# Optimization experiments

Hardware: AMD Instinct MI355X
Metric: run time of the kernel (lower is better)

## Reference

```python
import jax, jax.numpy as jnp
import numpy as np

B, H, S, D = 4, 16, 2048, 64
TEMPERATURE = 8.0  # sqrt(D)
MASK_FILL = -1e9


def setup_inputs() -> dict:
    key = jax.random.key(0)
    kq, kk, kv, km = jax.random.split(key, 4)
    q = jax.random.normal(kq, (B, H, S, D), dtype=jnp.float32)
    k = jax.random.normal(kk, (B, H, S, D), dtype=jnp.float32)
    v = jax.random.normal(kv, (B, H, S, D), dtype=jnp.float32)
    mask = jax.random.randint(km, (B, 1, 1, S), 0, 2, dtype=jnp.int32)
    return {"q": q, "k": k, "v": v, "mask": mask}


def reference(q, k, v, mask):
    # attn = (q / temperature) @ k^T  -> [B,H,S,S]
    attn = jnp.einsum('bhqd,bhkd->bhqk', q / TEMPERATURE, k)
    # mask-fill where mask == 0 (broadcasts over heads/query dim)
    attn = jnp.where(mask == 0, MASK_FILL, attn)
    # dropout is identity at inference (training=None in the original)
    # NOTE: the original module applies NO softmax; faithful reproduction.
    output = jnp.einsum('bhqk,bhkd->bhqd', attn, v)
    return (output, attn)
```

## Files before the change

### kernel.cpp

```cpp
#include <hip/hip_runtime.h>

constexpr int Bn = 4, Hn = 16, Sn = 2048, Dn = 64;
constexpr float MASK_FILL = -1e9f;
constexpr size_t KV_ELEMS = (size_t)Bn * Hn * Sn * Dn;

typedef __bf16 bf16x8 __attribute__((ext_vector_type(8)));
typedef __bf16 bf16x4 __attribute__((ext_vector_type(4)));
typedef float  f32x4  __attribute__((ext_vector_type(4)));
typedef int    i32x4  __attribute__((ext_vector_type(4)));

#define KSTRIDE 72
#define VSTRIDE 136

#define BARRIER_LGKM() asm volatile("s_waitcnt lgkmcnt(0)\n\ts_barrier" ::: "memory")

__global__ __launch_bounds__(256) void convert_kv(
    const float* __restrict__ kg, const float* __restrict__ vg,
    __bf16* __restrict__ kb, __bf16* __restrict__ vb)
{
  const size_t n4 = KV_ELEMS / 4;
  const size_t stride = (size_t)gridDim.x * 256;
  for (size_t i = (size_t)blockIdx.x * 256 + threadIdx.x; i < n4; i += stride) {
    f32x4 kv = __builtin_nontemporal_load((const f32x4*)(kg + i * 4));
    bf16x4 pk;
    pk.x = (__bf16)kv.x; pk.y = (__bf16)kv.y;
    pk.z = (__bf16)kv.z; pk.w = (__bf16)kv.w;
    *(bf16x4*)(kb + i * 4) = pk;
    f32x4 vv = __builtin_nontemporal_load((const f32x4*)(vg + i * 4));
    bf16x4 pv;
    pv.x = (__bf16)vv.x; pv.y = (__bf16)vv.y;
    pv.z = (__bf16)vv.z; pv.w = (__bf16)vv.w;
    *(bf16x4*)(vb + i * 4) = pv;
  }
}

template <bool PRE>
__global__ __launch_bounds__(256, 2) void attn_fused(
    const float* __restrict__ qg, const float* __restrict__ kg,
    const float* __restrict__ vg, const int* __restrict__ maskg,
    float* __restrict__ outg, float* __restrict__ attng,
    const __bf16* __restrict__ kbg, const __bf16* __restrict__ vbg)
{
  __shared__ __align__(16) __bf16 lds_k [128 * KSTRIDE];
  __shared__ __align__(16) __bf16 lds_vt[ 64 * VSTRIDE];
  __shared__ __align__(16) __bf16 lds_qs[128 * KSTRIDE];
  __shared__ __align__(16) int    lds_m [Sn];

  const int fid  = blockIdx.y * gridDim.x + blockIdx.x;
  const int nf   = ((fid & 7) << 7) | (fid >> 3);
  const int qt   = nf & 15;
  const int bh   = nf >> 4;
  const int b    = bh >> 4;
  const int tid  = threadIdx.x;
  const int wave = tid >> 6;
  const int lane = tid & 63;
  const int quad = lane >> 4;
  const int l16  = lane & 15;

  const int kt0  = nf & 15;

  const size_t hbase = (size_t)bh * Sn * Dn;
  const float* qp = qg + hbase + (size_t)qt * 128 * Dn;
  float* attnp = attng + (size_t)bh * Sn * Sn + (size_t)qt * 128 * (size_t)Sn;

  const int r0 = tid >> 4;
  const int c  = (tid & 15) << 2;

  {
    const int* mp = maskg + b * Sn;
    *(i32x4*)&lds_m[tid * 8]     = *(const i32x4*)(mp + tid * 8);
    *(i32x4*)&lds_m[tid * 8 + 4] = *(const i32x4*)(mp + tid * 8 + 4);
  }

#pragma unroll
  for (int i = 0; i < 8; ++i) {
    const int r = r0 + (i << 4);
    f32x4 val = __builtin_nontemporal_load((const f32x4*)(qp + r * Dn + c));
    bf16x4 pk;
    pk.x = (__bf16)(val.x * 0.125f);
    pk.y = (__bf16)(val.y * 0.125f);
    pk.z = (__bf16)(val.z * 0.125f);
    pk.w = (__bf16)(val.w * 0.125f);
    *(bf16x4*)&lds_qs[r * KSTRIDE + c] = pk;
  }

  f32x4  kpre [8], vpre [8];
  bf16x4 kpreb[8], vpreb[8];
  const float*  kbase  = kg  + hbase;
  const float*  vbase  = vg  + hbase;
  const __bf16* kbbase = PRE ? (kbg + hbase) : nullptr;
  const __bf16* vbbase = PRE ? (vbg + hbase) : nullptr;
  {
    const size_t toff = (size_t)(kt0 * 128) * Dn;
#pragma unroll
    for (int i = 0; i < 8; ++i) {
      if constexpr (PRE) {
        kpreb[i] = *(const bf16x4*)(kbbase + toff + (r0 + (i << 4)) * Dn + c);
        vpreb[i] = *(const bf16x4*)(vbbase + toff + (r0 * 8 + i) * Dn + c);
      } else {
        kpre[i] = *(const f32x4*)(kbase + toff + (r0 + (i << 4)) * Dn + c);
        vpre[i] = *(const f32x4*)(vbase + toff + (r0 * 8 + i) * Dn + c);
      }
    }
  }

  BARRIER_LGKM();

  bf16x8 qa[2][2];
#pragma unroll
  for (int qs = 0; qs < 2; ++qs)
#pragma unroll
    for (int ks = 0; ks < 2; ++ks)
      qa[qs][ks] = *(const bf16x8*)&lds_qs[(wave * 32 + qs * 16 + l16) * KSTRIDE + ks * 32 + quad * 8];

  __bf16* sbuf = &lds_qs[wave * 32 * KSTRIDE];

  f32x4 oacc[2][4];
#pragma unroll
  for (int qs = 0; qs < 2; ++qs)
#pragma unroll
    for (int ds = 0; ds < 4; ++ds)
      oacc[qs][ds] = (f32x4){0.f, 0.f, 0.f, 0.f};

  for (int it = 0; it < 16; ++it) {
    const int kt = (it + kt0) & 15;
    BARRIER_LGKM();

#pragma unroll
    for (int i = 0; i < 8; ++i) {
      const int r = r0 + (i << 4);
      if constexpr (PRE) {
        *(bf16x4*)&lds_k[r * KSTRIDE + c] = kpreb[i];
      } else {
        f32x4 kv = kpre[i];
        bf16x4 pk;
        pk.x = (__bf16)kv.x; pk.y = (__bf16)kv.y;
        pk.z = (__bf16)kv.z; pk.w = (__bf16)kv.w;
        *(bf16x4*)&lds_k[r * KSTRIDE + c] = pk;
      }
    }
#pragma unroll
    for (int j = 0; j < 4; ++j) {
      bf16x8 t;
#pragma unroll
      for (int i = 0; i < 8; ++i)
        t[i] = PRE ? vpreb[i][j] : (__bf16)vpre[i][j];
      *(bf16x8*)&lds_vt[(c + j) * VSTRIDE + r0 * 8] = t;
    }

    BARRIER_LGKM();

    if (it < 15) {
      const int ktn = (it + 1 + kt0) & 15;
      const size_t toff = (size_t)(ktn * 128) * Dn;
#pragma unroll
      for (int i = 0; i < 8; ++i) {
        if constexpr (PRE) {
          kpreb[i] = *(const bf16x4*)(kbbase + toff + (r0 + (i << 4)) * Dn + c);
          vpreb[i] = *(const bf16x4*)(vbbase + toff + (r0 * 8 + i) * Dn + c);
        } else {
          kpre[i] = *(const f32x4*)(kbase + toff + (r0 + (i << 4)) * Dn + c);
          vpre[i] = *(const f32x4*)(vbase + toff + (r0 * 8 + i) * Dn + c);
        }
      }
    }

    f32x4 sacc[2][8];
#pragma unroll
    for (int ns = 0; ns < 8; ++ns) {
      bf16x8 ka0 = *(const bf16x8*)&lds_k[(ns * 16 + l16) * KSTRIDE +      quad * 8];
      bf16x8 ka1 = *(const bf16x8*)&lds_k[(ns * 16 + l16) * KSTRIDE + 32 + quad * 8];
      const i32x4 m4 = *(const i32x4*)&lds_m[kt * 128 + ns * 16 + quad * 4];
#pragma unroll
      for (int qs = 0; qs < 2; ++qs) {
        f32x4 acc = (f32x4){0.f, 0.f, 0.f, 0.f};
        acc = __builtin_amdgcn_mfma_f32_16x16x32_bf16(ka0, qa[qs][0], acc, 0, 0, 0);
        acc = __builtin_amdgcn_mfma_f32_16x16x32_bf16(ka1, qa[qs][1], acc, 0, 0, 0);
        acc.x = m4.x ? acc.x : MASK_FILL;
        acc.y = m4.y ? acc.y : MASK_FILL;
        acc.z = m4.z ? acc.z : MASK_FILL;
        acc.w = m4.w ? acc.w : MASK_FILL;
        sacc[qs][ns] = acc;
        const int row = wave * 32 + qs * 16 + l16;
        *(f32x4*)(attnp + (size_t)row * Sn + kt * 128 + ns * 16 + quad * 4) = acc;
      }
    }

#pragma unroll
    for (int half = 0; half < 2; ++half) {
#pragma unroll
      for (int ns4 = 0; ns4 < 4; ++ns4) {
        const int ns = half * 4 + ns4;
#pragma unroll
        for (int qs = 0; qs < 2; ++qs) {
          f32x4 sv = sacc[qs][ns];
          bf16x4 sb;
          sb.x = (__bf16)sv.x; sb.y = (__bf16)sv.y;
          sb.z = (__bf16)sv.z; sb.w = (__bf16)sv.w;
          *(bf16x4*)&sbuf[(qs * 16 + l16) * KSTRIDE + ns4 * 16 + quad * 4] = sb;
        }
      }
      asm volatile("" ::: "memory");
#pragma unroll
      for (int ks = 0; ks < 2; ++ks) {
        bf16x8 sb0 = *(const bf16x8*)&sbuf[(     l16) * KSTRIDE + ks * 32 + quad * 8];
        bf16x8 sb1 = *(const bf16x8*)&sbuf[(16 + l16) * KSTRIDE + ks * 32 + quad * 8];
#pragma unroll
        for (int ds = 0; ds < 4; ++ds) {
          bf16x8 va = *(const bf16x8*)&lds_vt[(ds * 16 + l16) * VSTRIDE + half * 64 + ks * 32 + quad * 8];
          oacc[0][ds] = __builtin_amdgcn_mfma_f32_16x16x32_bf16(va, sb0, oacc[0][ds], 0, 0, 0);
          oacc[1][ds] = __builtin_amdgcn_mfma_f32_16x16x32_bf16(va, sb1, oacc[1][ds], 0, 0, 0);
        }
      }
      asm volatile("" ::: "memory");
    }
  }

  float* op = outg + hbase + (size_t)qt * 128 * Dn;
#pragma unroll
  for (int qs = 0; qs < 2; ++qs)
#pragma unroll
    for (int ds = 0; ds < 4; ++ds) {
      const int row = wave * 32 + qs * 16 + l16;
      __builtin_nontemporal_store(oacc[qs][ds],
          (f32x4*)(op + (size_t)row * Dn + ds * 16 + quad * 4));
    }
}

extern "C" void kernel_launch(void* const* d_in, const int* in_sizes, int n_in,
                              void* d_out, int out_size, void* d_ws, size_t ws_size,
                              hipStream_t stream) {
  const float* q    = (const float*)d_in[0];
  const float* k    = (const float*)d_in[1];
  const float* v    = (const float*)d_in[2];
  const int*   mask = (const int*)d_in[3];
  float* out  = (float*)d_out;
  float* attn = out + (size_t)Bn * Hn * Sn * Dn;

  dim3 grid(Sn / 128, Bn * Hn);
  const size_t need = KV_ELEMS * 2 * sizeof(__bf16);
  if (d_ws != nullptr && ws_size >= need) {
    __bf16* kb = (__bf16*)d_ws;
    __bf16* vb = kb + KV_ELEMS;
    convert_kv<<<2048, 256, 0, stream>>>(k, v, kb, vb);
    attn_fused<true><<<grid, 256, 0, stream>>>(q, k, v, mask, out, attn, kb, vb);
  } else {
    attn_fused<false><<<grid, 256, 0, stream>>>(q, k, v, mask, out, attn, nullptr, nullptr);
  }
}
```

Baseline: 1.184 ms.

## Pack mask to bitmask, drop mask LDS, interleave QK with PV per half

The int mask is packed into a 32-bit-per-word bitmask inside the conversion kernel. The attention kernel then reads one i32x4 per key tile instead of staging the whole mask in LDS. The score computation moves into the half loop, so only four score tiles are live at a time instead of holding sacc[2][8]. Launch bounds are raised to three blocks per SM. Together these cut register and LDS pressure to allow higher occupancy, at the risk of spills or worse MFMA scheduling.

```diff
diff --git a/kernel.cpp b/kernel.cpp
--- a/kernel.cpp
+++ b/kernel.cpp
@@ -8,6 +8,7 @@
 typedef __bf16 bf16x4 __attribute__((ext_vector_type(4)));
 typedef float  f32x4  __attribute__((ext_vector_type(4)));
 typedef int    i32x4  __attribute__((ext_vector_type(4)));
+typedef unsigned u32;
 
 #define KSTRIDE 72
 #define VSTRIDE 136
@@ -16,8 +17,23 @@
 
 __global__ __launch_bounds__(256) void convert_kv(
     const float* __restrict__ kg, const float* __restrict__ vg,
-    __bf16* __restrict__ kb, __bf16* __restrict__ vb)
+    const int* __restrict__ maskg,
+    __bf16* __restrict__ kb, __bf16* __restrict__ vb, u32* __restrict__ mb)
 {
+  if (blockIdx.x == 0) {
+    const int bb = threadIdx.x >> 6, w = threadIdx.x & 63;
+    const int* mp = maskg + bb * Sn + w * 32;
+    u32 bits = 0;
+#pragma unroll
+    for (int j = 0; j < 8; ++j) {
+      i32x4 m4 = *(const i32x4*)(mp + j * 4);
+      bits |= (m4.x != 0 ? 1u : 0u) << (j * 4 + 0);
+      bits |= (m4.y != 0 ? 1u : 0u) << (j * 4 + 1);
+      bits |= (m4.z != 0 ? 1u : 0u) << (j * 4 + 2);
+      bits |= (m4.w != 0 ? 1u : 0u) << (j * 4 + 3);
+    }
+    mb[bb * 64 + w] = bits;
+  }
   const size_t n4 = KV_ELEMS / 4;
   const size_t stride = (size_t)gridDim.x * 256;
   for (size_t i = (size_t)blockIdx.x * 256 + threadIdx.x; i < n4; i += stride) {
@@ -35,16 +51,16 @@
 }
 
 template <bool PRE>
-__global__ __launch_bounds__(256, 2) void attn_fused(
+__global__ __launch_bounds__(256, 3) void attn_fused(
     const float* __restrict__ qg, const float* __restrict__ kg,
     const float* __restrict__ vg, const int* __restrict__ maskg,
     float* __restrict__ outg, float* __restrict__ attng,
-    const __bf16* __restrict__ kbg, const __bf16* __restrict__ vbg)
+    const __bf16* __restrict__ kbg, const __bf16* __restrict__ vbg,
+    const u32* __restrict__ mbg)
 {
   __shared__ __align__(16) __bf16 lds_k [128 * KSTRIDE];
   __shared__ __align__(16) __bf16 lds_vt[ 64 * VSTRIDE];
   __shared__ __align__(16) __bf16 lds_qs[128 * KSTRIDE];
-  __shared__ __align__(16) int    lds_m [Sn];
 
   const int fid  = blockIdx.y * gridDim.x + blockIdx.x;
   const int nf   = ((fid & 7) << 7) | (fid >> 3);
@@ -66,12 +82,6 @@
   const int r0 = tid >> 4;
   const int c  = (tid & 15) << 2;
 
-  {
-    const int* mp = maskg + b * Sn;
-    *(i32x4*)&lds_m[tid * 8]     = *(const i32x4*)(mp + tid * 8);
-    *(i32x4*)&lds_m[tid * 8 + 4] = *(const i32x4*)(mp + tid * 8 + 4);
-  }
-
 #pragma unroll
   for (int i = 0; i < 8; ++i) {
     const int r = r0 + (i << 4);
@@ -150,6 +160,9 @@
 
     BARRIER_LGKM();
 
+    i32x4 mw;
+    if constexpr (PRE) mw = *(const i32x4*)(mbg + (b << 6) + (kt << 2));
+
     if (it < 15) {
       const int ktn = (it + 1 + kt0) & 15;
       const size_t toff = (size_t)(ktn * 128) * Dn;
@@ -165,38 +178,39 @@
       }
     }
 
-    f32x4 sacc[2][8];
-#pragma unroll
-    for (int ns = 0; ns < 8; ++ns) {
-      bf16x8 ka0 = *(const bf16x8*)&lds_k[(ns * 16 + l16) * KSTRIDE +      quad * 8];
-      bf16x8 ka1 = *(const bf16x8*)&lds_k[(ns * 16 + l16) * KSTRIDE + 32 + quad * 8];
-      const i32x4 m4 = *(const i32x4*)&lds_m[kt * 128 + ns * 16 + quad * 4];
-#pragma unroll
-      for (int qs = 0; qs < 2; ++qs) {
-        f32x4 acc = (f32x4){0.f, 0.f, 0.f, 0.f};
-        acc = __builtin_amdgcn_mfma_f32_16x16x32_bf16(ka0, qa[qs][0], acc, 0, 0, 0);
-        acc = __builtin_amdgcn_mfma_f32_16x16x32_bf16(ka1, qa[qs][1], acc, 0, 0, 0);
-        acc.x = m4.x ? acc.x : MASK_FILL;
-        acc.y = m4.y ? acc.y : MASK_FILL;
-        acc.z = m4.z ? acc.z : MASK_FILL;
-        acc.w = m4.w ? acc.w : MASK_FILL;
-        sacc[qs][ns] = acc;
-        const int row = wave * 32 + qs * 16 + l16;
-        *(f32x4*)(attnp + (size_t)row * Sn + kt * 128 + ns * 16 + quad * 4) = acc;
-      }
-    }
-
 #pragma unroll
     for (int half = 0; half < 2; ++half) {
 #pragma unroll
       for (int ns4 = 0; ns4 < 4; ++ns4) {
         const int ns = half * 4 + ns4;
+        bf16x8 ka0 = *(const bf16x8*)&lds_k[(ns * 16 + l16) * KSTRIDE +      quad * 8];
+        bf16x8 ka1 = *(const bf16x8*)&lds_k[(ns * 16 + l16) * KSTRIDE + 32 + quad * 8];
+        int bits;
+        if constexpr (PRE) {
+          bits = (int)(((u32)mw[ns >> 1]) >> (((ns & 1) << 4) | (quad << 2)));
+        }
 #pragma unroll
         for (int qs = 0; qs < 2; ++qs) {
-          f32x4 sv = sacc[qs][ns];
+          f32x4 acc = (f32x4){0.f, 0.f, 0.f, 0.f};
+          acc = __builtin_amdgcn_mfma_f32_16x16x32_bf16(ka0, qa[qs][0], acc, 0, 0, 0);
+          acc = __builtin_amdgcn_mfma_f32_16x16x32_bf16(ka1, qa[qs][1], acc, 0, 0, 0);
+          if constexpr (PRE) {
+            acc.x = (bits & 1) ? acc.x : MASK_FILL;
+            acc.y = (bits & 2) ? acc.y : MASK_FILL;
+            acc.z = (bits & 4) ? acc.z : MASK_FILL;
+            acc.w = (bits & 8) ? acc.w : MASK_FILL;
+          } else {
+            const i32x4 m4 = *(const i32x4*)(maskg + b * Sn + kt * 128 + ns * 16 + quad * 4);
+            acc.x = m4.x ? acc.x : MASK_FILL;
+            acc.y = m4.y ? acc.y : MASK_FILL;
+            acc.z = m4.z ? acc.z : MASK_FILL;
+            acc.w = m4.w ? acc.w : MASK_FILL;
+          }
+          const int row = wave * 32 + qs * 16 + l16;
+          *(f32x4*)(attnp + (size_t)row * Sn + kt * 128 + ns * 16 + quad * 4) = acc;
           bf16x4 sb;
-          sb.x = (__bf16)sv.x; sb.y = (__bf16)sv.y;
-          sb.z = (__bf16)sv.z; sb.w = (__bf16)sv.w;
+          sb.x = (__bf16)acc.x; sb.y = (__bf16)acc.y;
+          sb.z = (__bf16)acc.z; sb.w = (__bf16)acc.w;
           *(bf16x4*)&sbuf[(qs * 16 + l16) * KSTRIDE + ns4 * 16 + quad * 4] = sb;
         }
       }
@@ -238,13 +252,14 @@
   float* attn = out + (size_t)Bn * Hn * Sn * Dn;
 
   dim3 grid(Sn / 128, Bn * Hn);
-  const size_t need = KV_ELEMS * 2 * sizeof(__bf16);
+  const size_t need = KV_ELEMS * 2 * sizeof(__bf16) + 1024;
   if (d_ws != nullptr && ws_size >= need) {
     __bf16* kb = (__bf16*)d_ws;
     __bf16* vb = kb + KV_ELEMS;
-    convert_kv<<<2048, 256, 0, stream>>>(k, v, kb, vb);
-    attn_fused<true><<<grid, 256, 0, stream>>>(q, k, v, mask, out, attn, kb, vb);
+    u32*    mb = (u32*)(vb + KV_ELEMS);
+    convert_kv<<<2048, 256, 0, stream>>>(k, v, mask, kb, vb, mb);
+    attn_fused<true><<<grid, 256, 0, stream>>>(q, k, v, mask, out, attn, kb, vb, mb);
   } else {
-    attn_fused<false><<<grid, 256, 0, stream>>>(q, k, v, mask, out, attn, nullptr, nullptr);
+    attn_fused<false><<<grid, 256, 0, stream>>>(q, k, v, mask, out, attn, nullptr, nullptr, nullptr);
   }
 }
```

New measurement: 1.208 ms. 1.02x slower.

## Double query tile per block to 256 rows with 8 waves sharing K/V tiles

Applied to the files above, without the earlier changes.

Each block now handles 256 query rows using 512 threads, so every K/V tile staged in LDS is reused by twice as many query rows, halving K/V global traffic per output. The K and V prefetch is split across waves (waves 0-3 load K, waves 4-7 load V), which cuts per-thread prefetch registers. The QK^T MFMA is interleaved into the PV half-loop so the full score accumulator array no longer stays live, lowering register pressure. The risks are fewer blocks in the grid (512) and higher LDS use per block, which can reduce occupancy and load balance across CUs.

```diff
diff --git a/kernel.cpp b/kernel.cpp
--- a/kernel.cpp
+++ b/kernel.cpp
@@ -35,21 +35,21 @@
 }
 
 template <bool PRE>
-__global__ __launch_bounds__(256, 2) void attn_fused(
+__global__ __launch_bounds__(512, 4) void attn_fused(
     const float* __restrict__ qg, const float* __restrict__ kg,
     const float* __restrict__ vg, const int* __restrict__ maskg,
     float* __restrict__ outg, float* __restrict__ attng,
     const __bf16* __restrict__ kbg, const __bf16* __restrict__ vbg)
 {
+  __shared__ __align__(16) __bf16 lds_qs[256 * KSTRIDE];
   __shared__ __align__(16) __bf16 lds_k [128 * KSTRIDE];
   __shared__ __align__(16) __bf16 lds_vt[ 64 * VSTRIDE];
-  __shared__ __align__(16) __bf16 lds_qs[128 * KSTRIDE];
   __shared__ __align__(16) int    lds_m [Sn];
 
   const int fid  = blockIdx.y * gridDim.x + blockIdx.x;
-  const int nf   = ((fid & 7) << 7) | (fid >> 3);
-  const int qt   = nf & 15;
-  const int bh   = nf >> 4;
+  const int nf   = ((fid & 7) << 6) | (fid >> 3);
+  const int qt   = nf & 7;
+  const int bh   = nf >> 3;
   const int b    = bh >> 4;
   const int tid  = threadIdx.x;
   const int wave = tid >> 6;
@@ -60,21 +60,18 @@
   const int kt0  = nf & 15;
 
   const size_t hbase = (size_t)bh * Sn * Dn;
-  const float* qp = qg + hbase + (size_t)qt * 128 * Dn;
-  float* attnp = attng + (size_t)bh * Sn * Sn + (size_t)qt * 128 * (size_t)Sn;
-
-  const int r0 = tid >> 4;
-  const int c  = (tid & 15) << 2;
-
-  {
-    const int* mp = maskg + b * Sn;
-    *(i32x4*)&lds_m[tid * 8]     = *(const i32x4*)(mp + tid * 8);
-    *(i32x4*)&lds_m[tid * 8 + 4] = *(const i32x4*)(mp + tid * 8 + 4);
-  }
+  const float* qp = qg + hbase + (size_t)qt * 256 * Dn;
+  float* attnp = attng + (size_t)bh * Sn * Sn + (size_t)qt * 256 * (size_t)Sn;
+
+  const int r0q = tid >> 4;
+  const int r04 = r0q & 15;
+  const int c   = (tid & 15) << 2;
+
+  *(i32x4*)&lds_m[tid * 4] = *(const i32x4*)(maskg + b * Sn + tid * 4);
 
 #pragma unroll
   for (int i = 0; i < 8; ++i) {
-    const int r = r0 + (i << 4);
+    const int r = r0q + (i << 5);
     f32x4 val = __builtin_nontemporal_load((const f32x4*)(qp + r * Dn + c));
     bf16x4 pk;
     pk.x = (__bf16)(val.x * 0.125f);
@@ -84,8 +81,8 @@
     *(bf16x4*)&lds_qs[r * KSTRIDE + c] = pk;
   }
 
-  f32x4  kpre [8], vpre [8];
-  bf16x4 kpreb[8], vpreb[8];
+  f32x4  pre [8];
+  bf16x4 preb[8];
   const float*  kbase  = kg  + hbase;
   const float*  vbase  = vg  + hbase;
   const __bf16* kbbase = PRE ? (kbg + hbase) : nullptr;
@@ -94,12 +91,11 @@
     const size_t toff = (size_t)(kt0 * 128) * Dn;
 #pragma unroll
     for (int i = 0; i < 8; ++i) {
+      const int r = (wave < 4) ? (r04 + (i << 4)) : (r04 * 8 + i);
       if constexpr (PRE) {
-        kpreb[i] = *(const bf16x4*)(kbbase + toff + (r0 + (i << 4)) * Dn + c);
-        vpreb[i] = *(const bf16x4*)(vbbase + toff + (r0 * 8 + i) * Dn + c);
+        preb[i] = *(const bf16x4*)(((wave < 4) ? kbbase : vbbase) + toff + r * Dn + c);
       } else {
-        kpre[i] = *(const f32x4*)(kbase + toff + (r0 + (i << 4)) * Dn + c);
-        vpre[i] = *(const f32x4*)(vbase + toff + (r0 * 8 + i) * Dn + c);
+        pre[i] = *(const f32x4*)(((wave < 4) ? kbase : vbase) + toff + r * Dn + c);
       }
     }
   }
@@ -126,26 +122,29 @@
     const int kt = (it + kt0) & 15;
     BARRIER_LGKM();
 
-#pragma unroll
-    for (int i = 0; i < 8; ++i) {
-      const int r = r0 + (i << 4);
-      if constexpr (PRE) {
-        *(bf16x4*)&lds_k[r * KSTRIDE + c] = kpreb[i];
-      } else {
-        f32x4 kv = kpre[i];
-        bf16x4 pk;
-        pk.x = (__bf16)kv.x; pk.y = (__bf16)kv.y;
-        pk.z = (__bf16)kv.z; pk.w = (__bf16)kv.w;
-        *(bf16x4*)&lds_k[r * KSTRIDE + c] = pk;
-      }
-    }
-#pragma unroll
-    for (int j = 0; j < 4; ++j) {
-      bf16x8 t;
-#pragma unroll
-      for (int i = 0; i < 8; ++i)
-        t[i] = PRE ? vpreb[i][j] : (__bf16)vpre[i][j];
-      *(bf16x8*)&lds_vt[(c + j) * VSTRIDE + r0 * 8] = t;
+    if (wave < 4) {
+#pragma unroll
+      for (int i = 0; i < 8; ++i) {
+        const int r = r04 + (i << 4);
+        if constexpr (PRE) {
+          *(bf16x4*)&lds_k[r * KSTRIDE + c] = preb[i];
+        } else {
+          f32x4 kv = pre[i];
+          bf16x4 pk;
+          pk.x = (__bf16)kv.x; pk.y = (__bf16)kv.y;
+          pk.z = (__bf16)kv.z; pk.w = (__bf16)kv.w;
+          *(bf16x4*)&lds_k[r * KSTRIDE + c] = pk;
+        }
+      }
+    } else {
+#pragma unroll
+      for (int j = 0; j < 4; ++j) {
+        bf16x8 t;
+#pragma unroll
+        for (int i = 0; i < 8; ++i)
+          t[i] = PRE ? preb[i][j] : (__bf16)pre[i][j];
+        *(bf16x8*)&lds_vt[(c + j) * VSTRIDE + r04 * 8] = t;
+      }
     }
 
     BARRIER_LGKM();
@@ -155,34 +154,12 @@
       const size_t toff = (size_t)(ktn * 128) * Dn;
 #pragma unroll
       for (int i = 0; i < 8; ++i) {
+        const int r = (wave < 4) ? (r04 + (i << 4)) : (r04 * 8 + i);
         if constexpr (PRE) {
-          kpreb[i] = *(const bf16x4*)(kbbase + toff + (r0 + (i << 4)) * Dn + c);
-          vpreb[i] = *(const bf16x4*)(vbbase + toff + (r0 * 8 + i) * Dn + c);
+          preb[i] = *(const bf16x4*)(((wave < 4) ? kbbase : vbbase) + toff + r * Dn + c);
         } else {
-          kpre[i] = *(const f32x4*)(kbase + toff + (r0 + (i << 4)) * Dn + c);
-          vpre[i] = *(const f32x4*)(vbase + toff + (r0 * 8 + i) * Dn + c);
-        }
-      }
-    }
-
-    f32x4 sacc[2][8];
-#pragma unroll
-    for (int ns = 0; ns < 8; ++ns) {
-      bf16x8 ka0 = *(const bf16x8*)&lds_k[(ns * 16 + l16) * KSTRIDE +      quad * 8];
-      bf16x8 ka1 = *(const bf16x8*)&lds_k[(ns * 16 + l16) * KSTRIDE + 32 + quad * 8];
-      const i32x4 m4 = *(const i32x4*)&lds_m[kt * 128 + ns * 16 + quad * 4];
-#pragma unroll
-      for (int qs = 0; qs < 2; ++qs) {
-        f32x4 acc = (f32x4){0.f, 0.f, 0.f, 0.f};
-        acc = __builtin_amdgcn_mfma_f32_16x16x32_bf16(ka0, qa[qs][0], acc, 0, 0, 0);
-        acc = __builtin_amdgcn_mfma_f32_16x16x32_bf16(ka1, qa[qs][1], acc, 0, 0, 0);
-        acc.x = m4.x ? acc.x : MASK_FILL;
-        acc.y = m4.y ? acc.y : MASK_FILL;
-        acc.z = m4.z ? acc.z : MASK_FILL;
-        acc.w = m4.w ? acc.w : MASK_FILL;
-        sacc[qs][ns] = acc;
-        const int row = wave * 32 + qs * 16 + l16;
-        *(f32x4*)(attnp + (size_t)row * Sn + kt * 128 + ns * 16 + quad * 4) = acc;
+          pre[i] = *(const f32x4*)(((wave < 4) ? kbase : vbase) + toff + r * Dn + c);
+        }
       }
     }
 
@@ -191,12 +168,23 @@
 #pragma unroll
       for (int ns4 = 0; ns4 < 4; ++ns4) {
         const int ns = half * 4 + ns4;
+        bf16x8 ka0 = *(const bf16x8*)&lds_k[(ns * 16 + l16) * KSTRIDE +      quad * 8];
+        bf16x8 ka1 = *(const bf16x8*)&lds_k[(ns * 16 + l16) * KSTRIDE + 32 + quad * 8];
+        const i32x4 m4 = *(const i32x4*)&lds_m[kt * 128 + ns * 16 + quad * 4];
 #pragma unroll
         for (int qs = 0; qs < 2; ++qs) {
-          f32x4 sv = sacc[qs][ns];
+          f32x4 acc = (f32x4){0.f, 0.f, 0.f, 0.f};
+          acc = __builtin_amdgcn_mfma_f32_16x16x32_bf16(ka0, qa[qs][0], acc, 0, 0, 0);
+          acc = __builtin_amdgcn_mfma_f32_16x16x32_bf16(ka1, qa[qs][1], acc, 0, 0, 0);
+          acc.x = m4.x ? acc.x : MASK_FILL;
+          acc.y = m4.y ? acc.y : MASK_FILL;
+          acc.z = m4.z ? acc.z : MASK_FILL;
+          acc.w = m4.w ? acc.w : MASK_FILL;
+          const int row = wave * 32 + qs * 16 + l16;
+          *(f32x4*)(attnp + (size_t)row * Sn + kt * 128 + ns * 16 + quad * 4) = acc;
           bf16x4 sb;
-          sb.x = (__bf16)sv.x; sb.y = (__bf16)sv.y;
-          sb.z = (__bf16)sv.z; sb.w = (__bf16)sv.w;
+          sb.x = (__bf16)acc.x; sb.y = (__bf16)acc.y;
+          sb.z = (__bf16)acc.z; sb.w = (__bf16)acc.w;
           *(bf16x4*)&sbuf[(qs * 16 + l16) * KSTRIDE + ns4 * 16 + quad * 4] = sb;
         }
       }
@@ -216,7 +204,7 @@
     }
   }
 
-  float* op = outg + hbase + (size_t)qt * 128 * Dn;
+  float* op = outg + hbase + (size_t)qt * 256 * Dn;
 #pragma unroll
   for (int qs = 0; qs < 2; ++qs)
 #pragma unroll
@@ -237,14 +225,14 @@
   float* out  = (float*)d_out;
   float* attn = out + (size_t)Bn * Hn * Sn * Dn;
 
-  dim3 grid(Sn / 128, Bn * Hn);
+  dim3 grid(Sn / 256, Bn * Hn);
   const size_t need = KV_ELEMS * 2 * sizeof(__bf16);
   if (d_ws != nullptr && ws_size >= need) {
     __bf16* kb = (__bf16*)d_ws;
     __bf16* vb = kb + KV_ELEMS;
     convert_kv<<<2048, 256, 0, stream>>>(k, v, kb, vb);
-    attn_fused<true><<<grid, 256, 0, stream>>>(q, k, v, mask, out, attn, kb, vb);
+    attn_fused<true><<<grid, 512, 0, stream>>>(q, k, v, mask, out, attn, kb, vb);
   } else {
-    attn_fused<false><<<grid, 256, 0, stream>>>(q, k, v, mask, out, attn, nullptr, nullptr);
+    attn_fused<false><<<grid, 512, 0, stream>>>(q, k, v, mask, out, attn, nullptr, nullptr);
   }
 }
```

Result: slower. 1.242 ms (+4.9%).
